# Performance work log

Hardware: AMD Instinct MI355X
Metric: run time of the kernel (lower is better)

## Reference

```python
import jax, jax.numpy as jnp
import numpy as np

HIDDEN_DIM = 64
VOCAB_SIZE = 128
NUM_SLOTS = 64
B, L = 256, 4096


def layer_norm(x, gamma, beta, eps=1e-5):
    mu = jnp.mean(x, axis=-1, keepdims=True)
    var = jnp.mean(jnp.square(x - mu), axis=-1, keepdims=True)
    return (x - mu) * jax.lax.rsqrt(var + eps) * gamma + beta


def _l2norm(x, axis=-1, eps=1e-12):
    # matches torch F.normalize: x / max(||x||, eps)
    n = jnp.sqrt(jnp.sum(jnp.square(x), axis=axis, keepdims=True))
    return x / jnp.maximum(n, eps)


def setup_inputs() -> dict:
    key = jax.random.key(0)
    ks = jax.random.split(key, 13)
    H, V, S = HIDDEN_DIM, VOCAB_SIZE, NUM_SLOTS
    return {
        "seq": jax.random.randint(ks[0], (B, L), 0, V),
        "embed_w": jax.random.normal(ks[1], (V, H), dtype=jnp.float32),
        # linear weights stored [in, out] (transposed vs torch)
        "w1": jax.random.normal(ks[2], (H, 2 * H), dtype=jnp.float32) * 0.05,
        "b1": jnp.zeros((2 * H,), dtype=jnp.float32),
        "w2": jax.random.normal(ks[3], (2 * H, H), dtype=jnp.float32) * 0.05,
        "b2": jnp.zeros((H,), dtype=jnp.float32),
        "ln_g": jnp.ones((H,), dtype=jnp.float32),
        "ln_b": jnp.zeros((H,), dtype=jnp.float32),
        "slot_keys": jax.random.normal(ks[4], (S, H), dtype=jnp.float32) * 0.1,
        "slot_vals": jax.random.normal(ks[5], (S, H), dtype=jnp.float32) * 0.1,
        "gate_w": jax.random.normal(ks[6], (H, S), dtype=jnp.float32) * 0.05,
        "gate_b": jnp.zeros((S,), dtype=jnp.float32),
        "out_w": jax.random.normal(ks[7], (H, V), dtype=jnp.float32) * 0.05,
        "out_b": jnp.zeros((V,), dtype=jnp.float32),
    }


def reference(seq, embed_w, w1, b1, w2, b2, ln_g, ln_b,
              slot_keys, slot_vals, gate_w, gate_b, out_w, out_b):
    h = embed_w[seq]                                   # [B, L, H]
    ff = jnp.maximum(h @ w1 + b1, 0.0) @ w2 + b2       # [B, L, H]
    h = layer_norm(h + ff, ln_g, ln_b)

    hw = h[:, :-1, :]                                  # written tokens [B, L-1, H]
    w = jax.nn.softmax(hw @ gate_w + gate_b, axis=-1)  # [B, L-1, S]
    # the per-step increment w_t (outer) h_t is independent of prior keys,
    # so the sequential loop collapses exactly to one contraction:
    keys = slot_keys[None, :, :] + jnp.einsum('btn,bth->bnh', w, hw)  # [B, S, H]
    vals = keys  # loop sets vals = keys every step; L > 1 here

    q = h[:, -1, :]                                    # [B, H]
    sim = jnp.einsum('bnh,bh->bn', _l2norm(keys), _l2norm(q))
    attn = jax.nn.softmax(sim, axis=-1)                # [B, S]
    ctx = jnp.einsum('bn,bnh->bh', attn, vals)         # [B, H]
    return ctx @ out_w + out_b                         # [B, V]
```

## Files before the change

kernel.cpp:

```cpp
#include <hip/hip_runtime.h>

#define HD 64
#define VC 128
#define NS 64
#define NB 256
#define SL 4096

__device__ __forceinline__ float wsum(float x) {
#pragma unroll
  for (int o = 32; o > 0; o >>= 1) x += __shfl_xor(x, o, 64);
  return x;
}
__device__ __forceinline__ float wmax(float x) {
#pragma unroll
  for (int o = 32; o > 0; o >>= 1) x = fmaxf(x, __shfl_xor(x, o, 64));
  return x;
}

__global__ __launch_bounds__(128) void build_tables(
    const float* __restrict__ embed, const float* __restrict__ w1, const float* __restrict__ b1,
    const float* __restrict__ w2, const float* __restrict__ b2,
    const float* __restrict__ ln_g, const float* __restrict__ ln_b,
    const float* __restrict__ gate_w, const float* __restrict__ gate_b,
    float* __restrict__ HN, float* __restrict__ WSM)
{
  const int v = blockIdx.x, t = threadIdx.x;
  __shared__ float s_e[HD], s_f1[2 * HD], s_hn[HD];

  if (t < HD) s_e[t] = embed[v * HD + t];
  __syncthreads();

  float acc = b1[t];
  for (int h = 0; h < HD; ++h)
    acc = fmaf(s_e[h], w1[h * 2 * HD + t], acc);
  s_f1[t] = fmaxf(acc, 0.f);
  __syncthreads();

  if (t < HD) {
    float a2 = b2[t];
    for (int j = 0; j < 2 * HD; ++j)
      a2 = fmaf(s_f1[j], w2[j * HD + t], a2);
    float x = s_e[t] + a2;
    float mu = wsum(x) * (1.f / 64.f);
    float d = x - mu;
    float var = wsum(d * d) * (1.f / 64.f);
    float hn = d * rsqrtf(var + 1e-5f) * ln_g[t] + ln_b[t];
    s_hn[t] = hn;
    HN[v * HD + t] = hn;
  }
  __syncthreads();

  if (t < NS) {
    float g = gate_b[t];
    for (int h = 0; h < HD; ++h)
      g = fmaf(s_hn[h], gate_w[h * NS + t], g);
    float m = wmax(g);
    float e = expf(g - m);
    float s = wsum(e);
    WSM[v * NS + t] = e / s;
  }
}

__global__ __launch_bounds__(256) void batch_kernel(
    const int* __restrict__ seq, const float* __restrict__ HN, const float* __restrict__ WSM,
    const float* __restrict__ slot_keys, const float* __restrict__ out_w,
    const float* __restrict__ out_b, float* __restrict__ out)
{
  const int b = blockIdx.x, t = threadIdx.x;
  const int lane = t & 63, wave = t >> 6;

  __shared__ int s_cnt[VC];
  __shared__ int s_qtok;
  __align__(16) __shared__ float s_hn[64 * HD];
  __align__(16) __shared__ float s_wsm[64 * NS];
  __align__(16) __shared__ float s_keys[NS * HD];
  __shared__ float s_q[HD], s_sim[NS], s_attn[NS], s_ctx[HD];

  if (t < VC) s_cnt[t] = 0;
  __syncthreads();

  const int* sb = seq + b * SL;
  for (int i = t; i < SL - 1; i += 256) atomicAdd(&s_cnt[sb[i]], 1);
  if (t == 0) s_qtok = sb[SL - 1];
  __syncthreads();

  if (t < HD) s_q[t] = HN[s_qtok * HD + t];

  const int n0 = (t >> 4) << 2;
  const int h0 = (t & 15) << 2;
  float accv[4][4];
#pragma unroll
  for (int r = 0; r < 4; ++r)
#pragma unroll
    for (int c = 0; c < 4; ++c)
      accv[r][c] = slot_keys[(n0 + r) * HD + h0 + c];

  for (int p = 0; p < 2; ++p) {
    for (int i = t; i < 64 * HD; i += 256) {
      int v = (i >> 6) + (p << 6);
      s_hn[i] = HN[p * 64 * HD + i];
      s_wsm[i] = (float)s_cnt[v] * WSM[p * 64 * NS + i];
    }
    __syncthreads();
#pragma unroll 4
    for (int v = 0; v < 64; ++v) {
      const float4 hv = *(const float4*)&s_hn[v * HD + h0];
      const float4 wv = *(const float4*)&s_wsm[v * NS + n0];
      accv[0][0] = fmaf(wv.x, hv.x, accv[0][0]);
      accv[0][1] = fmaf(wv.x, hv.y, accv[0][1]);
      accv[0][2] = fmaf(wv.x, hv.z, accv[0][2]);
      accv[0][3] = fmaf(wv.x, hv.w, accv[0][3]);
      accv[1][0] = fmaf(wv.y, hv.x, accv[1][0]);
      accv[1][1] = fmaf(wv.y, hv.y, accv[1][1]);
      accv[1][2] = fmaf(wv.y, hv.z, accv[1][2]);
      accv[1][3] = fmaf(wv.y, hv.w, accv[1][3]);
      accv[2][0] = fmaf(wv.z, hv.x, accv[2][0]);
      accv[2][1] = fmaf(wv.z, hv.y, accv[2][1]);
      accv[2][2] = fmaf(wv.z, hv.z, accv[2][2]);
      accv[2][3] = fmaf(wv.z, hv.w, accv[2][3]);
      accv[3][0] = fmaf(wv.w, hv.x, accv[3][0]);
      accv[3][1] = fmaf(wv.w, hv.y, accv[3][1]);
      accv[3][2] = fmaf(wv.w, hv.z, accv[3][2]);
      accv[3][3] = fmaf(wv.w, hv.w, accv[3][3]);
    }
    __syncthreads();
  }

#pragma unroll
  for (int r = 0; r < 4; ++r) {
    float4 st;
    st.x = accv[r][0]; st.y = accv[r][1]; st.z = accv[r][2]; st.w = accv[r][3];
    *(float4*)&s_keys[(n0 + r) * HD + h0] = st;
  }
  __syncthreads();

  const float qv = s_q[lane];
  const float qn = fmaxf(sqrtf(wsum(qv * qv)), 1e-12f);
  for (int r = 0; r < 16; ++r) {
    const int n = wave * 16 + r;
    const float kv = s_keys[n * HD + lane];
    const float kk = wsum(kv * kv);
    const float kq = wsum(kv * qv);
    if (lane == 0) s_sim[n] = kq / (fmaxf(sqrtf(kk), 1e-12f) * qn);
  }
  __syncthreads();

  if (wave == 0) {
    float sv = s_sim[lane];
    float m = wmax(sv);
    float e = expf(sv - m);
    float ssum = wsum(e);
    s_attn[lane] = e / ssum;
  }
  __syncthreads();

  if (wave == 0) {
    float c = 0.f;
    for (int n = 0; n < NS; ++n) c = fmaf(s_attn[n], s_keys[n * HD + lane], c);
    s_ctx[lane] = c;
  }
  __syncthreads();

  if (t < VC) {
    float o = out_b[t];
    for (int h = 0; h < HD; ++h)
      o = fmaf(s_ctx[h], out_w[h * VC + t], o);
    out[b * VC + t] = o;
  }
}

extern "C" void kernel_launch(void* const* d_in, const int* in_sizes, int n_in,
                              void* d_out, int out_size, void* d_ws, size_t ws_size,
                              hipStream_t stream) {
  const int* seq         = (const int*)d_in[0];
  const float* embed_w   = (const float*)d_in[1];
  const float* w1        = (const float*)d_in[2];
  const float* b1        = (const float*)d_in[3];
  const float* w2        = (const float*)d_in[4];
  const float* b2        = (const float*)d_in[5];
  const float* ln_g      = (const float*)d_in[6];
  const float* ln_b      = (const float*)d_in[7];
  const float* slot_keys = (const float*)d_in[8];
  const float* gate_w    = (const float*)d_in[10];
  const float* gate_b    = (const float*)d_in[11];
  const float* out_w     = (const float*)d_in[12];
  const float* out_b     = (const float*)d_in[13];
  float* out = (float*)d_out;

  float* HN  = (float*)d_ws;
  float* WSM = HN + VC * HD;

  build_tables<<<VC, 128, 0, stream>>>(embed_w, w1, b1, w2, b2, ln_g, ln_b,
                                       gate_w, gate_b, HN, WSM);
  batch_kernel<<<NB, 256, 0, stream>>>(seq, HN, WSM, slot_keys, out_w, out_b, out);
}
```

Baseline: 105.2 us.

## Double batch block size, split vocab contraction across halves, stage tables once

The batch kernel now runs 512 threads per block. Both 64-token halves of the HN/WSM tables are loaded into shared memory in one vectorized pass, and each half of the block contracts one of them. The two partial key matrices are then combined in shared memory. The histogram, similarity, and context reduction are also spread over the eight waves. This is meant to cut the serial two-pass contraction and barrier count per block and to improve latency hiding during the seq read. The cost is doubled shared memory (about 80KB per block), which may limit occupancy, plus an extra reduction step.

```diff
diff --git a/kernel.cpp b/kernel.cpp
--- a/kernel.cpp
+++ b/kernel.cpp
@@ -31,6 +31,7 @@
   __syncthreads();
 
   float acc = b1[t];
+#pragma unroll 8
   for (int h = 0; h < HD; ++h)
     acc = fmaf(s_e[h], w1[h * 2 * HD + t], acc);
   s_f1[t] = fmaxf(acc, 0.f);
@@ -38,6 +39,7 @@
 
   if (t < HD) {
     float a2 = b2[t];
+#pragma unroll 8
     for (int j = 0; j < 2 * HD; ++j)
       a2 = fmaf(s_f1[j], w2[j * HD + t], a2);
     float x = s_e[t] + a2;
@@ -52,6 +54,7 @@
 
   if (t < NS) {
     float g = gate_b[t];
+#pragma unroll 8
     for (int h = 0; h < HD; ++h)
       g = fmaf(s_hn[h], gate_w[h * NS + t], g);
     float m = wmax(g);
@@ -61,7 +64,7 @@
   }
 }
 
-__global__ __launch_bounds__(256) void batch_kernel(
+__global__ __launch_bounds__(512) void batch_kernel(
     const int* __restrict__ seq, const float* __restrict__ HN, const float* __restrict__ WSM,
     const float* __restrict__ slot_keys, const float* __restrict__ out_w,
     const float* __restrict__ out_b, float* __restrict__ out)
@@ -71,73 +74,100 @@
 
   __shared__ int s_cnt[VC];
   __shared__ int s_qtok;
-  __align__(16) __shared__ float s_hn[64 * HD];
-  __align__(16) __shared__ float s_wsm[64 * NS];
+  __align__(16) __shared__ float s_hn[VC * HD];
+  __align__(16) __shared__ float s_wsm[VC * NS];
   __align__(16) __shared__ float s_keys[NS * HD];
+  __shared__ float s_part[8 * HD];
   __shared__ float s_q[HD], s_sim[NS], s_attn[NS], s_ctx[HD];
 
   if (t < VC) s_cnt[t] = 0;
   __syncthreads();
 
   const int* sb = seq + b * SL;
-  for (int i = t; i < SL - 1; i += 256) atomicAdd(&s_cnt[sb[i]], 1);
+  for (int i = t; i < SL - 1; i += 512) atomicAdd(&s_cnt[sb[i]], 1);
   if (t == 0) s_qtok = sb[SL - 1];
-  __syncthreads();
-
-  if (t < HD) s_q[t] = HN[s_qtok * HD + t];
-
-  const int n0 = (t >> 4) << 2;
-  const int h0 = (t & 15) << 2;
+#pragma unroll
+  for (int i4 = t; i4 < VC * HD / 4; i4 += 512)
+    ((float4*)s_hn)[i4] = ((const float4*)HN)[i4];
+  __syncthreads();
+
+  if (t < HD) s_q[t] = s_hn[s_qtok * HD + t];
+#pragma unroll
+  for (int i4 = t; i4 < VC * NS / 4; i4 += 512) {
+    float4 wv = ((const float4*)WSM)[i4];
+    const float c = (float)s_cnt[i4 >> 4];
+    wv.x *= c; wv.y *= c; wv.z *= c; wv.w *= c;
+    ((float4*)s_wsm)[i4] = wv;
+  }
+  __syncthreads();
+
+  const int tid = t & 255;
+  const int half = t >> 8;
+  const int n0 = (tid >> 4) << 2;
+  const int h0 = (tid & 15) << 2;
+  const float* hbase = s_hn + half * 64 * HD;
+  const float* wbase = s_wsm + half * 64 * NS;
+
   float accv[4][4];
-#pragma unroll
-  for (int r = 0; r < 4; ++r)
-#pragma unroll
-    for (int c = 0; c < 4; ++c)
-      accv[r][c] = slot_keys[(n0 + r) * HD + h0 + c];
-
-  for (int p = 0; p < 2; ++p) {
-    for (int i = t; i < 64 * HD; i += 256) {
-      int v = (i >> 6) + (p << 6);
-      s_hn[i] = HN[p * 64 * HD + i];
-      s_wsm[i] = (float)s_cnt[v] * WSM[p * 64 * NS + i];
-    }
-    __syncthreads();
+  if (half == 0) {
+#pragma unroll
+    for (int r = 0; r < 4; ++r) {
+      const float4 sk = *(const float4*)&slot_keys[(n0 + r) * HD + h0];
+      accv[r][0] = sk.x; accv[r][1] = sk.y; accv[r][2] = sk.z; accv[r][3] = sk.w;
+    }
+  } else {
+#pragma unroll
+    for (int r = 0; r < 4; ++r)
+#pragma unroll
+      for (int c = 0; c < 4; ++c) accv[r][c] = 0.f;
+  }
+
 #pragma unroll 4
-    for (int v = 0; v < 64; ++v) {
-      const float4 hv = *(const float4*)&s_hn[v * HD + h0];
-      const float4 wv = *(const float4*)&s_wsm[v * NS + n0];
-      accv[0][0] = fmaf(wv.x, hv.x, accv[0][0]);
-      accv[0][1] = fmaf(wv.x, hv.y, accv[0][1]);
-      accv[0][2] = fmaf(wv.x, hv.z, accv[0][2]);
-      accv[0][3] = fmaf(wv.x, hv.w, accv[0][3]);
-      accv[1][0] = fmaf(wv.y, hv.x, accv[1][0]);
-      accv[1][1] = fmaf(wv.y, hv.y, accv[1][1]);
-      accv[1][2] = fmaf(wv.y, hv.z, accv[1][2]);
-      accv[1][3] = fmaf(wv.y, hv.w, accv[1][3]);
-      accv[2][0] = fmaf(wv.z, hv.x, accv[2][0]);
-      accv[2][1] = fmaf(wv.z, hv.y, accv[2][1]);
-      accv[2][2] = fmaf(wv.z, hv.z, accv[2][2]);
-      accv[2][3] = fmaf(wv.z, hv.w, accv[2][3]);
-      accv[3][0] = fmaf(wv.w, hv.x, accv[3][0]);
-      accv[3][1] = fmaf(wv.w, hv.y, accv[3][1]);
-      accv[3][2] = fmaf(wv.w, hv.z, accv[3][2]);
-      accv[3][3] = fmaf(wv.w, hv.w, accv[3][3]);
-    }
-    __syncthreads();
-  }
-
-#pragma unroll
-  for (int r = 0; r < 4; ++r) {
-    float4 st;
-    st.x = accv[r][0]; st.y = accv[r][1]; st.z = accv[r][2]; st.w = accv[r][3];
-    *(float4*)&s_keys[(n0 + r) * HD + h0] = st;
+  for (int v = 0; v < 64; ++v) {
+    const float4 hv = *(const float4*)&hbase[v * HD + h0];
+    const float4 wv = *(const float4*)&wbase[v * NS + n0];
+    accv[0][0] = fmaf(wv.x, hv.x, accv[0][0]);
+    accv[0][1] = fmaf(wv.x, hv.y, accv[0][1]);
+    accv[0][2] = fmaf(wv.x, hv.z, accv[0][2]);
+    accv[0][3] = fmaf(wv.x, hv.w, accv[0][3]);
+    accv[1][0] = fmaf(wv.y, hv.x, accv[1][0]);
+    accv[1][1] = fmaf(wv.y, hv.y, accv[1][1]);
+    accv[1][2] = fmaf(wv.y, hv.z, accv[1][2]);
+    accv[1][3] = fmaf(wv.y, hv.w, accv[1][3]);
+    accv[2][0] = fmaf(wv.z, hv.x, accv[2][0]);
+    accv[2][1] = fmaf(wv.z, hv.y, accv[2][1]);
+    accv[2][2] = fmaf(wv.z, hv.z, accv[2][2]);
+    accv[2][3] = fmaf(wv.z, hv.w, accv[2][3]);
+    accv[3][0] = fmaf(wv.w, hv.x, accv[3][0]);
+    accv[3][1] = fmaf(wv.w, hv.y, accv[3][1]);
+    accv[3][2] = fmaf(wv.w, hv.z, accv[3][2]);
+    accv[3][3] = fmaf(wv.w, hv.w, accv[3][3]);
+  }
+  __syncthreads();
+
+  if (half == 1) {
+#pragma unroll
+    for (int r = 0; r < 4; ++r) {
+      float4 st; st.x = accv[r][0]; st.y = accv[r][1]; st.z = accv[r][2]; st.w = accv[r][3];
+      *(float4*)&s_keys[(n0 + r) * HD + h0] = st;
+    }
+  }
+  __syncthreads();
+  if (half == 0) {
+#pragma unroll
+    for (int r = 0; r < 4; ++r) {
+      float4 p = *(const float4*)&s_keys[(n0 + r) * HD + h0];
+      p.x += accv[r][0]; p.y += accv[r][1]; p.z += accv[r][2]; p.w += accv[r][3];
+      *(float4*)&s_keys[(n0 + r) * HD + h0] = p;
+    }
   }
   __syncthreads();
 
   const float qv = s_q[lane];
   const float qn = fmaxf(sqrtf(wsum(qv * qv)), 1e-12f);
-  for (int r = 0; r < 16; ++r) {
-    const int n = wave * 16 + r;
+#pragma unroll
+  for (int r = 0; r < 8; ++r) {
+    const int n = wave * 8 + r;
     const float kv = s_keys[n * HD + lane];
     const float kk = wsum(kv * kv);
     const float kq = wsum(kv * qv);
@@ -154,15 +184,27 @@
   }
   __syncthreads();
 
+  {
+    float c = 0.f;
+#pragma unroll
+    for (int r = 0; r < 8; ++r) {
+      const int n = wave * 8 + r;
+      c = fmaf(s_attn[n], s_keys[n * HD + lane], c);
+    }
+    s_part[wave * HD + lane] = c;
+  }
+  __syncthreads();
   if (wave == 0) {
     float c = 0.f;
-    for (int n = 0; n < NS; ++n) c = fmaf(s_attn[n], s_keys[n * HD + lane], c);
+#pragma unroll
+    for (int w = 0; w < 8; ++w) c += s_part[w * HD + lane];
     s_ctx[lane] = c;
   }
   __syncthreads();
 
   if (t < VC) {
     float o = out_b[t];
+#pragma unroll 8
     for (int h = 0; h < HD; ++h)
       o = fmaf(s_ctx[h], out_w[h * VC + t], o);
     out[b * VC + t] = o;
@@ -192,5 +234,5 @@
 
   build_tables<<<VC, 128, 0, stream>>>(embed_w, w1, b1, w2, b2, ln_g, ln_b,
                                        gate_w, gate_b, HN, WSM);
-  batch_kernel<<<NB, 256, 0, stream>>>(seq, HN, WSM, slot_keys, out_w, out_b, out);
-}
+  batch_kernel<<<NB, 512, 0, stream>>>(seq, HN, WSM, slot_keys, out_w, out_b, out);
+}
```

Measured after the change: 103.4 us. About the same (-1.6%).
